# Kernel optimization log

Hardware: AMD Instinct MI355X
Metric: run time of the kernel (lower is better)

Reference implementation:

```python
import jax, jax.numpy as jnp
import numpy as np

WINDOW = 64
BAND_NUM = 2 * WINDOW      # 128
FILTER_LEN = 6 * WINDOW    # 384


def setup_inputs() -> dict:
    key = jax.random.key(0)
    k1, k2 = jax.random.split(key)
    B, C, T, F = 16, 1, 8192, WINDOW + 1  # F = band_num/2 + 1 = 65
    inp = jax.random.normal(k1, (B, C, T, F), dtype=jnp.float32)
    subband_filter = jax.random.normal(k2, (FILTER_LEN,), dtype=jnp.float32)
    lengths = jnp.full((B,), T, dtype=jnp.int32)  # one sample per batch element, all length T
    return {"input": inp, "subband_filter": subband_filter, "lengths": lengths}


def reference(input, subband_filter, lengths):
    B, C, T, F = input.shape
    S = lengths.shape[0]               # sample_num (static)
    x = input.reshape(-1, F)           # (N, F), N = B*C*T
    # torch.fft.irfft(norm='forward') -> jnp.fft.irfft(norm='forward'), out len = 2*(F-1) = band_num
    ifft_out = jnp.fft.irfft(x, norm='forward')          # (N, 128)
    # tile across the 3 band repeats, apply prototype filter and window gain
    wide = jnp.concatenate([ifft_out, ifft_out, ifft_out], axis=1)  # (N, 384)
    wide = wide * subband_filter[None, :] * WINDOW
    N = wide.shape[0]
    H = N // S                          # in_height (= C*T per sample)
    w = wide.reshape(S, H, 6, WINDOW)   # per-sample, per-frame, 6 taps of width `window`
    true_len = H - 5
    # overlap-add: out[s, t] = sum_k w[s, t + 5 - k, k]
    out = w[:, 5:H, 0, :]
    for k in range(1, 6):
        out = out + w[:, 5 - k:H - k, k, :]
    out = out.reshape(B, C, -1)         # (B, C, true_len*window)
    return out / 32768.0
```

## Files before the change

kernel.cpp:

```cpp
#include <hip/hip_runtime.h>
#include <hip/hip_bf16.h>


#define NF 65
#define NT 8192
#define TRUE_LEN 8187
#define FPW 59
#define CPB 139
#define XSTR 67
#define TSTR 36
#define EOSTR 34
#define YSTR 66

typedef const __attribute__((address_space(4))) float cfloat;

__device__ float d_tab[2 * 33 * TSTR];

__global__ void build_tab_kernel() {
    int idx = blockIdx.x * 256 + threadIdx.x;
    if (idx >= 2 * 33 * TSTR) return;
    int par = idx / (33 * TSTR);
    int rem = idx - par * 33 * TSTR;
    int p = rem / TSTR, n = rem - p * TSTR;
    int m = 2 * n + par;
    float v = 0.0f;
    if (n < 33 && m <= 64) {
        float w = (m == 0 || m == 64) ? 1.0f : 2.0f;
        int a = (m * p) & 127;
        v = w * cospif((float)a * (1.0f / 64.0f));
    }
    d_tab[idx] = v;
}

__global__ __launch_bounds__(128, 4)
void subband_main_kernel(const float* __restrict__ g_in,
                         const float* __restrict__ g_filt,
                         float* __restrict__ g_out)
{
    __shared__ float smem[64 * XSTR];
    __hip_bfloat16* Es = (__hip_bfloat16*)smem;
    __hip_bfloat16* Os = (__hip_bfloat16*)((char*)smem + 4352);
    __hip_bfloat16* Yb = (__hip_bfloat16*)((char*)smem + 8704);

    const int tid  = threadIdx.x;
    const int lane = tid & 63;
    const int wv   = tid >> 6;
    const int cg   = blockIdx.x;
    const int s     = cg / CPB;
    const int fbase = (cg - s * CPB) * FPW;

    const float* src = g_in + (size_t)s * NT * NF;
    for (int i = tid; i < 64 * NF; i += 128) {
        int r = i / NF, c = i - r * NF;
        int h = fbase + r; if (h > NT - 1) h = NT - 1;
        smem[r * XSTR + c] = src[(size_t)h * NF + c];
    }
    { int r = tid >> 1, sl = NF + (tid & 1); smem[r * XSTR + sl] = 0.0f; }
    __syncthreads();

    const int row = lane;
    float Xr[33];
    #pragma unroll
    for (int n = 0; n < 33; ++n) Xr[n] = smem[row * XSTR + 2 * n + wv];
    __syncthreads();

    const int tab_off = __builtin_amdgcn_readfirstlane(wv * (33 * TSTR));
    cfloat* ct = (cfloat*)(unsigned long long)(const float*)(d_tab + tab_off);
    __hip_bfloat16* eo = (wv == 0) ? Es : Os;
    for (int p = 0; p < 33; ++p) {
        cfloat* cf = ct + p * TSTR;
        float a0 = 0.0f, a1 = 0.0f, a2 = 0.0f, a3 = 0.0f;
        #pragma unroll
        for (int n = 0; n < 32; n += 4) {
            a0 += cf[n]     * Xr[n];
            a1 += cf[n + 1] * Xr[n + 1];
            a2 += cf[n + 2] * Xr[n + 2];
            a3 += cf[n + 3] * Xr[n + 3];
        }
        a0 += cf[32] * Xr[32];
        eo[row * EOSTR + p] = __float2bfloat16((a0 + a2) + (a1 + a3));
    }
    __syncthreads();

    {
        const int crow = wv * 32 + (lane & 31);
        const int g = lane >> 5;
        for (int it = 0; it < 17; ++it) {
            const int q = g * 17 + it;
            if (q > 32) break;
            const int t0 = 2 * q, t1 = 2 * q + 1;
            const int p0 = (t0 <= 32) ? t0 : 64 - t0;
            const float e0 = __bfloat162float(Es[crow * EOSTR + p0]);
            const float o0 = __bfloat162float(Os[crow * EOSTR + p0]);
            const float y0 = (t0 <= 32) ? e0 + o0 : e0 - o0;
            float y1 = 0.0f;
            if (t1 <= 64) {
                const int p1 = (t1 <= 32) ? t1 : 64 - t1;
                const float e1 = __bfloat162float(Es[crow * EOSTR + p1]);
                const float o1 = __bfloat162float(Os[crow * EOSTR + p1]);
                y1 = (t1 <= 32) ? e1 + o1 : e1 - o1;
            }
            __hip_bfloat162 pk;
            pk.x = __float2bfloat16(y0);
            pk.y = __float2bfloat16(y1);
            *(__hip_bfloat162*)&Yb[crow * YSTR + t0] = pk;
        }
    }
    __syncthreads();

    const int j = lane;
    float fc[6];
    #pragma unroll
    for (int k = 0; k < 6; ++k) fc[k] = g_filt[k * 64 + j] * (1.0f / 512.0f);
    const int te = j;
    const int to = (j == 0) ? 64 : 64 - j;
    const int qlo = wv * 30;
    const int nq  = 30 - wv;

    float we[6], wo[6];
    #pragma unroll
    for (int r = 0; r < 5; ++r) {
        we[r] = __bfloat162float(Yb[(qlo + r) * YSTR + te]);
        wo[r] = __bfloat162float(Yb[(qlo + r) * YSTR + to]);
    }
    float* dst = g_out + ((size_t)s * TRUE_LEN + fbase + qlo) * 64 + j;

    for (int u = 0; u < nq; ++u) {
        if (fbase + qlo + u >= TRUE_LEN) break;
        we[5] = __bfloat162float(Yb[(qlo + u + 5) * YSTR + te]);
        wo[5] = __bfloat162float(Yb[(qlo + u + 5) * YSTR + to]);
        const float o = fc[0] * we[5] + fc[1] * wo[4] + fc[2] * we[3]
                      + fc[3] * wo[2] + fc[4] * we[1] + fc[5] * wo[0];
        dst[(size_t)u * 64] = o;
        #pragma unroll
        for (int r = 0; r < 5; ++r) { we[r] = we[r + 1]; wo[r] = wo[r + 1]; }
    }
}

extern "C" void kernel_launch(void* const* d_in, const int* in_sizes, int n_in,
                              void* d_out, int out_size, void* d_ws, size_t ws_size,
                              hipStream_t stream) {
    const float* g_in   = (const float*)d_in[0];
    const float* g_filt = (const float*)d_in[1];
    float* g_out = (float*)d_out;

    build_tab_kernel<<<10, 256, 0, stream>>>();
    subband_main_kernel<<<16 * CPB, 128, 0, stream>>>(g_in, g_filt, g_out);
}
```

Before: 105.8 us.

## Load input via global_load_lds and fuse even/odd DFT into symmetric output writes

Input rows are now copied straight from global memory into LDS with the global_load_lds builtin in 16-byte chunks, with a scalar fallback for the tail block. Instead of each wave computing one parity half over 33 frequencies, each wave keeps all 65 coefficients in registers and handles half of the output indices. For each index it forms the even and odd partial sums and writes both y[p] and y[64-p] directly. This drops the intermediate E/O buffers and their combine pass, at the cost of more registers per thread (65 values held) and an LDS layout with no padding.

```diff
diff --git a/kernel.cpp b/kernel.cpp
--- a/kernel.cpp
+++ b/kernel.cpp
@@ -7,24 +7,21 @@
 #define TRUE_LEN 8187
 #define FPW 59
 #define CPB 139
-#define XSTR 67
-#define TSTR 36
-#define EOSTR 34
+#define TSTR 68
 #define YSTR 66
 
 typedef const __attribute__((address_space(4))) float cfloat;
+typedef __attribute__((address_space(1))) const void gv_t;
+typedef __attribute__((address_space(3))) void lv_t;
 
-__device__ float d_tab[2 * 33 * TSTR];
+__device__ float d_tab[33 * TSTR];
 
 __global__ void build_tab_kernel() {
     int idx = blockIdx.x * 256 + threadIdx.x;
-    if (idx >= 2 * 33 * TSTR) return;
-    int par = idx / (33 * TSTR);
-    int rem = idx - par * 33 * TSTR;
-    int p = rem / TSTR, n = rem - p * TSTR;
-    int m = 2 * n + par;
+    if (idx >= 33 * TSTR) return;
+    int p = idx / TSTR, m = idx - p * TSTR;
     float v = 0.0f;
-    if (n < 33 && m <= 64) {
+    if (m < NF) {
         float w = (m == 0 || m == 64) ? 1.0f : 2.0f;
         int a = (m * p) & 127;
         v = w * cospif((float)a * (1.0f / 64.0f));
@@ -32,15 +29,20 @@
     d_tab[idx] = v;
 }
 
+__device__ __forceinline__ void gl_lds16(const float* g, float* l) {
+    __builtin_amdgcn_global_load_lds((gv_t*)g, (lv_t*)l, 16, 0, 0);
+}
+__device__ __forceinline__ void gl_lds4(const float* g, float* l) {
+    __builtin_amdgcn_global_load_lds((gv_t*)g, (lv_t*)l, 4, 0, 0);
+}
+
 __global__ __launch_bounds__(128, 4)
 void subband_main_kernel(const float* __restrict__ g_in,
                          const float* __restrict__ g_filt,
                          float* __restrict__ g_out)
 {
-    __shared__ float smem[64 * XSTR];
-    __hip_bfloat16* Es = (__hip_bfloat16*)smem;
-    __hip_bfloat16* Os = (__hip_bfloat16*)((char*)smem + 4352);
-    __hip_bfloat16* Yb = (__hip_bfloat16*)((char*)smem + 8704);
+    __shared__ float smem[64 * NF];
+    __hip_bfloat16* Yb = (__hip_bfloat16*)smem;
 
     const int tid  = threadIdx.x;
     const int lane = tid & 63;
@@ -49,62 +51,45 @@
     const int s     = cg / CPB;
     const int fbase = (cg - s * CPB) * FPW;
 
-    const float* src = g_in + (size_t)s * NT * NF;
-    for (int i = tid; i < 64 * NF; i += 128) {
-        int r = i / NF, c = i - r * NF;
-        int h = fbase + r; if (h > NT - 1) h = NT - 1;
-        smem[r * XSTR + c] = src[(size_t)h * NF + c];
-    }
-    { int r = tid >> 1, sl = NF + (tid & 1); smem[r * XSTR + sl] = 0.0f; }
-    __syncthreads();
-
-    const int row = lane;
-    float Xr[33];
-    #pragma unroll
-    for (int n = 0; n < 33; ++n) Xr[n] = smem[row * XSTR + 2 * n + wv];
-    __syncthreads();
-
-    const int tab_off = __builtin_amdgcn_readfirstlane(wv * (33 * TSTR));
-    cfloat* ct = (cfloat*)(unsigned long long)(const float*)(d_tab + tab_off);
-    __hip_bfloat16* eo = (wv == 0) ? Es : Os;
-    for (int p = 0; p < 33; ++p) {
-        cfloat* cf = ct + p * TSTR;
-        float a0 = 0.0f, a1 = 0.0f, a2 = 0.0f, a3 = 0.0f;
-        #pragma unroll
-        for (int n = 0; n < 32; n += 4) {
-            a0 += cf[n]     * Xr[n];
-            a1 += cf[n + 1] * Xr[n + 1];
-            a2 += cf[n + 2] * Xr[n + 2];
-            a3 += cf[n + 3] * Xr[n + 3];
+    if (fbase + 64 <= NT) {
+        const float* src = g_in + ((size_t)s * NT + fbase) * NF;
+        for (int c = wv; c < 16; c += 2)
+            gl_lds16(src + c * 256 + lane * 4, smem + c * 256);
+        if (wv == 0)
+            gl_lds4(src + 4096 + lane, smem + 4096);
+    } else {
+        const float* src = g_in + (size_t)s * NT * NF;
+        for (int i = tid; i < 64 * NF; i += 128) {
+            int r = i / NF, c = i - r * NF;
+            int h = fbase + r; if (h > NT - 1) h = NT - 1;
+            smem[i] = src[(size_t)h * NF + c];
         }
-        a0 += cf[32] * Xr[32];
-        eo[row * EOSTR + p] = __float2bfloat16((a0 + a2) + (a1 + a3));
     }
     __syncthreads();
 
-    {
-        const int crow = wv * 32 + (lane & 31);
-        const int g = lane >> 5;
-        for (int it = 0; it < 17; ++it) {
-            const int q = g * 17 + it;
-            if (q > 32) break;
-            const int t0 = 2 * q, t1 = 2 * q + 1;
-            const int p0 = (t0 <= 32) ? t0 : 64 - t0;
-            const float e0 = __bfloat162float(Es[crow * EOSTR + p0]);
-            const float o0 = __bfloat162float(Os[crow * EOSTR + p0]);
-            const float y0 = (t0 <= 32) ? e0 + o0 : e0 - o0;
-            float y1 = 0.0f;
-            if (t1 <= 64) {
-                const int p1 = (t1 <= 32) ? t1 : 64 - t1;
-                const float e1 = __bfloat162float(Es[crow * EOSTR + p1]);
-                const float o1 = __bfloat162float(Os[crow * EOSTR + p1]);
-                y1 = (t1 <= 32) ? e1 + o1 : e1 - o1;
-            }
-            __hip_bfloat162 pk;
-            pk.x = __float2bfloat16(y0);
-            pk.y = __float2bfloat16(y1);
-            *(__hip_bfloat162*)&Yb[crow * YSTR + t0] = pk;
+    float X[NF];
+    #pragma unroll
+    for (int m = 0; m < NF; ++m) X[m] = smem[lane * NF + m];
+    __syncthreads();
+
+    const int pbase = wv * 17;
+    const int pcnt  = 17 - wv;
+    cfloat* ct = (cfloat*)(unsigned long long)(const float*)d_tab;
+    for (int pp = 0; pp < pcnt; ++pp) {
+        const int p = pbase + pp;
+        cfloat* cf = ct + p * TSTR;
+        float e0 = 0.0f, e1 = 0.0f, o0 = 0.0f, o1 = 0.0f;
+        #pragma unroll
+        for (int m = 0; m < 64; m += 4) {
+            e0 += cf[m]     * X[m];
+            o0 += cf[m + 1] * X[m + 1];
+            e1 += cf[m + 2] * X[m + 2];
+            o1 += cf[m + 3] * X[m + 3];
         }
+        e0 += cf[64] * X[64];
+        const float E = e0 + e1, O = o0 + o1;
+        Yb[lane * YSTR + p]      = __float2bfloat16(E + O);
+        Yb[lane * YSTR + 64 - p] = __float2bfloat16(E - O);
     }
     __syncthreads();
 
@@ -144,6 +129,6 @@
     const float* g_filt = (const float*)d_in[1];
     float* g_out = (float*)d_out;
 
-    build_tab_kernel<<<10, 256, 0, stream>>>();
+    build_tab_kernel<<<9, 256, 0, stream>>>();
     subband_main_kernel<<<16 * CPB, 128, 0, stream>>>(g_in, g_filt, g_out);
 }
```

Measured after the change: 122.6 us. 1.16x slower.

## Load input tile via global_load_lds and double threads per block to 256

Applied to the files above, without the earlier changes.

Replaces the per-element strided global-to-LDS copy with direct global_load_lds 16-byte transfers of the contiguous 64x65 input tile, dropping the padded row stride. The block grows from two to four waves, splitting the DCT-style matmul, the symmetric combine, and the overlap-add output rows across the extra waves. This aims to cut load latency and raise per-block parallelism. In exchange it adds LDS bank conflicts from the odd unpadded stride (65) on row reads, and more register/occupancy pressure at 256 threads.

```diff
diff --git a/kernel.cpp b/kernel.cpp
--- a/kernel.cpp
+++ b/kernel.cpp
@@ -7,12 +7,13 @@
 #define TRUE_LEN 8187
 #define FPW 59
 #define CPB 139
-#define XSTR 67
 #define TSTR 36
 #define EOSTR 34
 #define YSTR 66
 
 typedef const __attribute__((address_space(4))) float cfloat;
+typedef __attribute__((address_space(1))) const void gv_t;
+typedef __attribute__((address_space(3))) void lv_t;
 
 __device__ float d_tab[2 * 33 * TSTR];
 
@@ -32,79 +33,94 @@
     d_tab[idx] = v;
 }
 
-__global__ __launch_bounds__(128, 4)
+__device__ __forceinline__ void gl_lds16(const float* g, float* l) {
+    __builtin_amdgcn_global_load_lds((gv_t*)g, (lv_t*)l, 16, 0, 0);
+}
+__device__ __forceinline__ void gl_lds4(const float* g, float* l) {
+    __builtin_amdgcn_global_load_lds((gv_t*)g, (lv_t*)l, 4, 0, 0);
+}
+
+__global__ __launch_bounds__(256, 8)
 void subband_main_kernel(const float* __restrict__ g_in,
                          const float* __restrict__ g_filt,
                          float* __restrict__ g_out)
 {
-    __shared__ float smem[64 * XSTR];
+    __shared__ float smem[64 * 67];
     __hip_bfloat16* Es = (__hip_bfloat16*)smem;
-    __hip_bfloat16* Os = (__hip_bfloat16*)((char*)smem + 4352);
+    __hip_bfloat16* Os = Es + 64 * EOSTR;
     __hip_bfloat16* Yb = (__hip_bfloat16*)((char*)smem + 8704);
 
     const int tid  = threadIdx.x;
     const int lane = tid & 63;
     const int wv   = tid >> 6;
+    const int par  = wv & 1;
+    const int ph   = wv >> 1;
     const int cg   = blockIdx.x;
     const int s     = cg / CPB;
     const int fbase = (cg - s * CPB) * FPW;
 
-    const float* src = g_in + (size_t)s * NT * NF;
-    for (int i = tid; i < 64 * NF; i += 128) {
-        int r = i / NF, c = i - r * NF;
-        int h = fbase + r; if (h > NT - 1) h = NT - 1;
-        smem[r * XSTR + c] = src[(size_t)h * NF + c];
-    }
-    { int r = tid >> 1, sl = NF + (tid & 1); smem[r * XSTR + sl] = 0.0f; }
-    __syncthreads();
-
-    const int row = lane;
-    float Xr[33];
-    #pragma unroll
-    for (int n = 0; n < 33; ++n) Xr[n] = smem[row * XSTR + 2 * n + wv];
-    __syncthreads();
-
-    const int tab_off = __builtin_amdgcn_readfirstlane(wv * (33 * TSTR));
-    cfloat* ct = (cfloat*)(unsigned long long)(const float*)(d_tab + tab_off);
-    __hip_bfloat16* eo = (wv == 0) ? Es : Os;
-    for (int p = 0; p < 33; ++p) {
-        cfloat* cf = ct + p * TSTR;
-        float a0 = 0.0f, a1 = 0.0f, a2 = 0.0f, a3 = 0.0f;
-        #pragma unroll
-        for (int n = 0; n < 32; n += 4) {
-            a0 += cf[n]     * Xr[n];
-            a1 += cf[n + 1] * Xr[n + 1];
-            a2 += cf[n + 2] * Xr[n + 2];
-            a3 += cf[n + 3] * Xr[n + 3];
+    if (fbase + 64 <= NT) {
+        const float* src = g_in + ((size_t)s * NT + fbase) * NF;
+        for (int c = wv; c < 16; c += 4)
+            gl_lds16(src + c * 256 + lane * 4, smem + c * 256);
+        if (wv == 0)
+            gl_lds4(src + 4096 + lane, smem + 4096);
+    } else {
+        const float* src = g_in + (size_t)s * NT * NF;
+        for (int i = tid; i < 64 * NF; i += 256) {
+            int r = i / NF, c = i - r * NF;
+            int h = fbase + r; if (h > NT - 1) h = NT - 1;
+            smem[i] = src[(size_t)h * NF + c];
         }
-        a0 += cf[32] * Xr[32];
-        eo[row * EOSTR + p] = __float2bfloat16((a0 + a2) + (a1 + a3));
     }
     __syncthreads();
 
+    float Xr[33];
+    #pragma unroll
+    for (int n = 0; n < 32; ++n) Xr[n] = smem[lane * NF + 2 * n + par];
+    Xr[32] = (par == 0) ? smem[lane * NF + 64] : 0.0f;
+    __syncthreads();
+
     {
-        const int crow = wv * 32 + (lane & 31);
-        const int g = lane >> 5;
-        for (int it = 0; it < 17; ++it) {
-            const int q = g * 17 + it;
-            if (q > 32) break;
-            const int t0 = 2 * q, t1 = 2 * q + 1;
-            const int p0 = (t0 <= 32) ? t0 : 64 - t0;
-            const float e0 = __bfloat162float(Es[crow * EOSTR + p0]);
-            const float o0 = __bfloat162float(Os[crow * EOSTR + p0]);
-            const float y0 = (t0 <= 32) ? e0 + o0 : e0 - o0;
-            float y1 = 0.0f;
-            if (t1 <= 64) {
-                const int p1 = (t1 <= 32) ? t1 : 64 - t1;
-                const float e1 = __bfloat162float(Es[crow * EOSTR + p1]);
-                const float o1 = __bfloat162float(Os[crow * EOSTR + p1]);
-                y1 = (t1 <= 32) ? e1 + o1 : e1 - o1;
+        const int tbase = __builtin_amdgcn_readfirstlane(
+            par * (33 * TSTR) + ph * (17 * TSTR));
+        cfloat* ct = (cfloat*)(unsigned long long)(const float*)(d_tab + tbase);
+        __hip_bfloat16* eo = (par == 0) ? Es : Os;
+        const int pcnt = 17 - ph;
+        for (int pp = 0; pp < pcnt; ++pp) {
+            cfloat* cf = ct + pp * TSTR;
+            float a0 = 0.0f, a1 = 0.0f, a2 = 0.0f, a3 = 0.0f;
+            #pragma unroll
+            for (int n = 0; n < 32; n += 4) {
+                a0 += cf[n]     * Xr[n];
+                a1 += cf[n + 1] * Xr[n + 1];
+                a2 += cf[n + 2] * Xr[n + 2];
+                a3 += cf[n + 3] * Xr[n + 3];
             }
-            __hip_bfloat162 pk;
-            pk.x = __float2bfloat16(y0);
-            pk.y = __float2bfloat16(y1);
-            *(__hip_bfloat162*)&Yb[crow * YSTR + t0] = pk;
+            a0 += cf[32] * Xr[32];
+            eo[lane * EOSTR + ph * 17 + pp] =
+                __float2bfloat16((a0 + a2) + (a1 + a3));
         }
+    }
+    __syncthreads();
+
+    for (int q = wv; q <= 32; q += 4) {
+        const int t0 = 2 * q, t1 = 2 * q + 1;
+        const int p0 = (t0 <= 32) ? t0 : 64 - t0;
+        const float e0 = __bfloat162float(Es[lane * EOSTR + p0]);
+        const float o0 = __bfloat162float(Os[lane * EOSTR + p0]);
+        const float y0 = (t0 <= 32) ? e0 + o0 : e0 - o0;
+        float y1 = 0.0f;
+        if (t1 <= 64) {
+            const int p1 = (t1 <= 32) ? t1 : 64 - t1;
+            const float e1 = __bfloat162float(Es[lane * EOSTR + p1]);
+            const float o1 = __bfloat162float(Os[lane * EOSTR + p1]);
+            y1 = (t1 <= 32) ? e1 + o1 : e1 - o1;
+        }
+        __hip_bfloat162 pk;
+        pk.x = __float2bfloat16(y0);
+        pk.y = __float2bfloat16(y1);
+        *(__hip_bfloat162*)&Yb[lane * YSTR + t0] = pk;
     }
     __syncthreads();
 
@@ -114,8 +130,8 @@
     for (int k = 0; k < 6; ++k) fc[k] = g_filt[k * 64 + j] * (1.0f / 512.0f);
     const int te = j;
     const int to = (j == 0) ? 64 : 64 - j;
-    const int qlo = wv * 30;
-    const int nq  = 30 - wv;
+    const int qlo = wv * 15;
+    const int nq  = (wv == 3) ? 14 : 15;
 
     float we[6], wo[6];
     #pragma unroll
@@ -145,5 +161,5 @@
     float* g_out = (float*)d_out;
 
     build_tab_kernel<<<10, 256, 0, stream>>>();
-    subband_main_kernel<<<16 * CPB, 128, 0, stream>>>(g_in, g_filt, g_out);
+    subband_main_kernel<<<16 * CPB, 256, 0, stream>>>(g_in, g_filt, g_out);
 }
```

Measured after the change: 150.3 us. +42.1%, slower.
